# Performance work log

Measured on AMD Instinct MI355X. Metric: run time of the kernel, lower is better.

## Reference

```python
import jax, jax.numpy as jnp
import numpy as np

B, T, D, H = 2, 2048, 1024, 16
HD = D // H
DFF = 4 * D
EPS = 1e-5


def gelu_tanh(x):
    c = jnp.sqrt(2.0 / jnp.pi).astype(x.dtype)
    return 0.5 * x * (1.0 + jnp.tanh(c * (x + 0.044715 * x ** 3)))


def layernorm(x, scale, shift):
    mean = jnp.mean(x, axis=-1, keepdims=True)
    var = jnp.var(x, axis=-1, keepdims=True)  # unbiased=False
    return (x - mean) / jnp.sqrt(var + EPS) * scale + shift


def setup_inputs() -> dict:
    key = jax.random.key(0)
    ks = jax.random.split(key, 12)
    s = lambda fan_in: 1.0 / np.sqrt(fan_in)
    return {
        "x": jax.random.normal(ks[0], (B, T, D), jnp.float32),
        "wq": jax.random.normal(ks[1], (D, D), jnp.float32) * s(D),
        "wk": jax.random.normal(ks[2], (D, D), jnp.float32) * s(D),
        "wv": jax.random.normal(ks[3], (D, D), jnp.float32) * s(D),
        "wo": jax.random.normal(ks[4], (D, D), jnp.float32) * s(D),
        "bo": jnp.zeros((D,), jnp.float32),
        "ln1_scale": jnp.ones((D,), jnp.float32),
        "ln1_shift": jnp.zeros((D,), jnp.float32),
        "ln2_scale": jnp.ones((D,), jnp.float32),
        "ln2_shift": jnp.zeros((D,), jnp.float32),
        "w1": jax.random.normal(ks[5], (D, DFF), jnp.float32) * s(D),
        "b1": jnp.zeros((DFF,), jnp.float32),
        "w2": jax.random.normal(ks[6], (DFF, D), jnp.float32) * s(DFF),
        "b2": jnp.zeros((D,), jnp.float32),
    }


def reference(x, wq, wk, wv, wo, bo, ln1_scale, ln1_shift, ln2_scale, ln2_shift, w1, b1, w2, b2):
    # pre-LN attention
    h = layernorm(x, ln1_scale, ln1_shift)
    q = (h @ wq).reshape(B, T, H, HD).transpose(0, 2, 1, 3)  # [B,H,T,hd]
    k = (h @ wk).reshape(B, T, H, HD).transpose(0, 2, 1, 3)
    v = (h @ wv).reshape(B, T, H, HD).transpose(0, 2, 1, 3)
    scores = jnp.einsum('bhqd,bhkd->bhqk', q, k) / jnp.sqrt(jnp.float32(HD))
    causal = jnp.tril(jnp.ones((T, T), bool))
    scores = jnp.where(causal, scores, -jnp.inf)
    attn = jax.nn.softmax(scores, axis=-1)
    ctx = jnp.einsum('bhqk,bhkd->bhqd', attn, v)
    ctx = ctx.transpose(0, 2, 1, 3).reshape(B, T, D)
    attn_out = ctx @ wo + bo
    x = x + attn_out  # dropout p=0
    # pre-LN FFN
    h2 = layernorm(x, ln2_scale, ln2_shift)
    ff = gelu_tanh(h2 @ w1 + b1) @ w2 + b2
    return x + ff
```

## Files before the change

kernel.cpp:

```cpp
#include <hip/hip_runtime.h>
#include <hip/hip_bf16.h>
#include <stdint.h>

typedef unsigned short u16;
typedef __attribute__((ext_vector_type(8))) short s16x8;
typedef __attribute__((ext_vector_type(4))) float f32x4;

#define B_   2
#define T_   2048
#define D_   1024
#define H_   16
#define HD_  64
#define DFF_ 4096
#define M_   (B_*T_)

#define SC2F 0.18033688f

__device__ __forceinline__ u16 f2b(float f){
  uint32_t u = __float_as_uint(f);
  u += 0x7FFFu + ((u >> 16) & 1u);
  return (u16)(u >> 16);
}
__device__ __forceinline__ uint32_t pk2(float lo, float hi){
  uint32_t r;
  asm volatile("v_cvt_pk_bf16_f32 %0, %1, %2" : "=v"(r) : "v"(lo), "v"(hi));
  return r;
}

__device__ __forceinline__ void gl_lds16(const void* g, void* l){
  __builtin_amdgcn_global_load_lds((const __attribute__((address_space(1))) void*)g,
                                   (__attribute__((address_space(3))) void*)l, 16, 0, 0);
}

#define WAITV4 asm volatile("s_waitcnt vmcnt(4)" ::: "memory")
#define WAITV0 asm volatile("s_waitcnt vmcnt(0)" ::: "memory")
#define BARRIER do{ asm volatile("":::"memory"); __builtin_amdgcn_s_barrier(); \
                    asm volatile("":::"memory"); }while(0)

__global__ __launch_bounds__(256) void wconv_all(const float* __restrict__ wq,
                                                 const float* __restrict__ wk,
                                                 const float* __restrict__ wv,
                                                 const float* __restrict__ wo,
                                                 const float* __restrict__ w1,
                                                 const float* __restrict__ w2,
                                                 u16* __restrict__ wqkvT, u16* __restrict__ woT,
                                                 u16* __restrict__ w1T,   u16* __restrict__ w2T){
  const int bid = blockIdx.x;
  const float* W; u16* Wt; int K, N, tk, tn;
  if (bid < 1024){
    const int which = bid >> 8, t = bid & 255; tk = t >> 4; tn = t & 15; K = 1024; N = 1024;
    W  = (which == 0) ? wq : (which == 1) ? wk : (which == 2) ? wv : wo;
    Wt = (which == 3) ? woT : wqkvT + (size_t)which * D_ * D_;
  } else if (bid < 2048){
    const int t = bid - 1024; tk = t >> 6; tn = t & 63; K = 1024; N = 4096; W = w1; Wt = w1T;
  } else {
    const int t = bid - 2048; tk = t >> 4; tn = t & 15; K = 4096; N = 1024; W = w2; Wt = w2T;
  }
  const int k0 = tk << 6, n0 = tn << 6;
  __shared__ u16 tile[64][68];
  const int tid = threadIdx.x;
  const int rr = tid >> 4, c4 = (tid & 15) << 2;
  #pragma unroll
  for (int rep = 0; rep < 4; rep++){
    int r = rr + (rep << 4);
    float4 v = *reinterpret_cast<const float4*>(W + (size_t)(k0 + r)*N + n0 + c4);
    tile[r][c4+0] = f2b(v.x); tile[r][c4+1] = f2b(v.y);
    tile[r][c4+2] = f2b(v.z); tile[r][c4+3] = f2b(v.w);
  }
  __syncthreads();
  const int rn = tid >> 2, kb = (tid & 3) << 4;
  u16 tmp[16];
  #pragma unroll
  for (int j = 0; j < 16; j++) tmp[j] = tile[kb + j][rn];
  ushort4* dst = reinterpret_cast<ushort4*>(Wt + (size_t)(n0 + rn)*K + k0 + kb);
  dst[0] = make_ushort4(tmp[0], tmp[1], tmp[2], tmp[3]);
  dst[1] = make_ushort4(tmp[4], tmp[5], tmp[6], tmp[7]);
  dst[2] = make_ushort4(tmp[8], tmp[9], tmp[10], tmp[11]);
  dst[3] = make_ushort4(tmp[12], tmp[13], tmp[14], tmp[15]);
}

__global__ __launch_bounds__(256) void ln_kernel(const float* __restrict__ X,
                                                 const float* __restrict__ sc,
                                                 const float* __restrict__ sh,
                                                 u16* __restrict__ out){
  const int row = blockIdx.x;
  const int tid = threadIdx.x;
  float4 a = reinterpret_cast<const float4*>(X + ((size_t)row << 10))[tid];
  float s = a.x + a.y + a.z + a.w;
  float q = a.x*a.x + a.y*a.y + a.z*a.z + a.w*a.w;
  #pragma unroll
  for (int o = 32; o > 0; o >>= 1){ s += __shfl_xor(s, o); q += __shfl_xor(q, o); }
  __shared__ float red[8];
  const int w = tid >> 6;
  if ((tid & 63) == 0){ red[w] = s; red[4 + w] = q; }
  __syncthreads();
  float S = red[0] + red[1] + red[2] + red[3];
  float Q = red[4] + red[5] + red[6] + red[7];
  float mean = S * (1.0f/1024.0f);
  float var  = Q * (1.0f/1024.0f) - mean*mean;
  float inv = rsqrtf(var + 1e-5f);
  float4 gsc = reinterpret_cast<const float4*>(sc)[tid];
  float4 gsh = reinterpret_cast<const float4*>(sh)[tid];
  ushort4 o4;
  o4.x = f2b((a.x - mean)*inv*gsc.x + gsh.x);
  o4.y = f2b((a.y - mean)*inv*gsc.y + gsh.y);
  o4.z = f2b((a.z - mean)*inv*gsc.z + gsh.z);
  o4.w = f2b((a.w - mean)*inv*gsc.w + gsh.w);
  reinterpret_cast<ushort4*>(out + ((size_t)row << 10))[tid] = o4;
}

__global__ __launch_bounds__(256) void reduce2(const float* __restrict__ p,
                                               const float* __restrict__ bias,
                                               const float* __restrict__ resid,
                                               float* __restrict__ out){
  const size_t idx = ((size_t)blockIdx.x << 8) + threadIdx.x;
  float4 a = reinterpret_cast<const float4*>(p)[idx];
  float4 b = reinterpret_cast<const float4*>(p)[idx + (((size_t)M_*D_) >> 2)];
  float4 r = reinterpret_cast<const float4*>(resid)[idx];
  float4 bb = reinterpret_cast<const float4*>(bias)[threadIdx.x];
  float4 o;
  o.x = a.x + b.x + r.x + bb.x;
  o.y = a.y + b.y + r.y + bb.y;
  o.z = a.z + b.z + r.z + bb.z;
  o.w = a.w + b.w + r.w + bb.w;
  reinterpret_cast<float4*>(out)[idx] = o;
}

__global__ __launch_bounds__(256) void reduce_ln(const float* __restrict__ p,
                                                 const float* __restrict__ bias,
                                                 const float* __restrict__ resid,
                                                 const float* __restrict__ sc,
                                                 const float* __restrict__ sh,
                                                 float* __restrict__ x1,
                                                 u16* __restrict__ h2){
  const int row = blockIdx.x;
  const int tid = threadIdx.x;
  const size_t idx = ((size_t)row << 8) + tid;
  float4 a  = reinterpret_cast<const float4*>(p)[idx];
  float4 b  = reinterpret_cast<const float4*>(p)[idx + (((size_t)M_*D_) >> 2)];
  float4 r  = reinterpret_cast<const float4*>(resid)[idx];
  float4 bb = reinterpret_cast<const float4*>(bias)[tid];
  float4 v;
  v.x = a.x + b.x + r.x + bb.x;
  v.y = a.y + b.y + r.y + bb.y;
  v.z = a.z + b.z + r.z + bb.z;
  v.w = a.w + b.w + r.w + bb.w;
  reinterpret_cast<float4*>(x1)[idx] = v;
  float s = v.x + v.y + v.z + v.w;
  float q = v.x*v.x + v.y*v.y + v.z*v.z + v.w*v.w;
  #pragma unroll
  for (int o = 32; o > 0; o >>= 1){ s += __shfl_xor(s, o); q += __shfl_xor(q, o); }
  __shared__ float red[8];
  const int w = tid >> 6;
  if ((tid & 63) == 0){ red[w] = s; red[4 + w] = q; }
  __syncthreads();
  float S = red[0] + red[1] + red[2] + red[3];
  float Q = red[4] + red[5] + red[6] + red[7];
  float mean = S * (1.0f/1024.0f);
  float var  = Q * (1.0f/1024.0f) - mean*mean;
  float inv = rsqrtf(var + 1e-5f);
  float4 gsc = reinterpret_cast<const float4*>(sc)[tid];
  float4 gsh = reinterpret_cast<const float4*>(sh)[tid];
  ushort4 o4;
  o4.x = f2b((v.x - mean)*inv*gsc.x + gsh.x);
  o4.y = f2b((v.y - mean)*inv*gsc.y + gsh.y);
  o4.z = f2b((v.z - mean)*inv*gsc.z + gsh.z);
  o4.w = f2b((v.w - mean)*inv*gsc.w + gsh.w);
  reinterpret_cast<ushort4*>(h2 + ((size_t)row << 10))[tid] = o4;
}

template<int EPI>
__global__ __launch_bounds__(256) void gemm_k(const u16* __restrict__ A, const u16* __restrict__ Bt,
                                              const float* __restrict__ bias,
                                              void* __restrict__ Cv, int M, int N, int K, int lda){
  __shared__ __align__(16) u16 As[2][128*32];
  __shared__ __align__(16) u16 Bs[2][128*32];
  const int tid = threadIdx.x;
  const int lane = tid & 63;
  const int w = tid >> 6;
  const int wr = w >> 1, wc = w & 1;
  const int g = lane >> 4, l15 = lane & 15;

  const int nx = gridDim.x, ny = gridDim.y;
  const int nwg = nx * ny * gridDim.z;
  const int flat = blockIdx.x + nx * (blockIdx.y + ny * blockIdx.z);
  const int nf = (flat & 7) * (nwg >> 3) + (flat >> 3);
  const int tn = nf % nx;
  const int rest = nf / nx;
  const int tm = rest % ny;
  const int kz = rest / ny;
  const int tn0 = tn << 7;
  const int tm0 = tm << 7;
  const u16* Az = A  + (size_t)kz * K;
  const u16* Bz = Bt + (size_t)kz * K;

  f32x4 acc[4][4];
  #pragma unroll
  for (int i = 0; i < 4; i++)
    #pragma unroll
    for (int j = 0; j < 4; j++) acc[i][j] = (f32x4){0.f,0.f,0.f,0.f};

  const int ch0 = tid, ch1 = 256 + tid;
  const int r0 = ch0 >> 2, c0 = (((ch0 & 3) ^ ((r0 >> 1) & 3)) << 3);
  const int r1 = ch1 >> 2, c1 = (((ch1 & 3) ^ ((r1 >> 1) & 3)) << 3);
  const u16* A0 = Az + (size_t)(tm0 + r0)*lda + c0;
  const u16* A1 = Az + (size_t)(tm0 + r1)*lda + c1;
  const u16* B0 = Bz + (size_t)(tn0 + r0)*lda + c0;
  const u16* B1 = Bz + (size_t)(tn0 + r1)*lda + c1;

#define GSTAGE(BUF, TI) do {                         \
    const int off_ = (TI) << 5;                      \
    gl_lds16(A0 + off_, As[BUF] + ch0*8);            \
    gl_lds16(A1 + off_, As[BUF] + ch1*8);            \
    gl_lds16(B0 + off_, Bs[BUF] + ch0*8);            \
    gl_lds16(B1 + off_, Bs[BUF] + ch1*8);            \
  } while(0)

#define GCOMP(BUF) do {                                                                   \
    s16x8 af[4], bf[4];                                                                   \
    _Pragma("unroll")                                                                     \
    for (int i = 0; i < 4; i++){                                                          \
      int ra = (wr << 6) + (i << 4) + l15;                                                \
      af[i] = *reinterpret_cast<const s16x8*>(As[BUF] + ra*32 + ((g ^ ((ra >> 1) & 3)) << 3)); \
    }                                                                                     \
    _Pragma("unroll")                                                                     \
    for (int j = 0; j < 4; j++){                                                          \
      int rb = (wc << 6) + (j << 4) + l15;                                                \
      bf[j] = *reinterpret_cast<const s16x8*>(Bs[BUF] + rb*32 + ((g ^ ((rb >> 1) & 3)) << 3)); \
    }                                                                                     \
    _Pragma("unroll")                                                                     \
    for (int i = 0; i < 4; i++)                                                           \
      _Pragma("unroll")                                                                   \
      for (int j = 0; j < 4; j++)                                                         \
        acc[i][j] = __builtin_amdgcn_mfma_f32_16x16x32_bf16(af[i], bf[j], acc[i][j], 0, 0, 0); \
  } while(0)

  const int NT = K >> 5;
  GSTAGE(0, 0);
  for (int t = 0; t < NT; t += 2){
    if (t + 1 < NT) { GSTAGE(1, t + 1); WAITV4; } else { WAITV0; }
    BARRIER;
    GCOMP(0);
    BARRIER;
    if (t + 2 < NT) { GSTAGE(0, t + 2); WAITV4; } else { WAITV0; }
    BARRIER;
    GCOMP(1);
    BARRIER;
  }
#undef GSTAGE
#undef GCOMP

  #pragma unroll
  for (int i = 0; i < 4; i++){
    const int mb = tm0 + (wr << 6) + (i << 4) + (g << 2);
    #pragma unroll
    for (int j = 0; j < 4; j++){
      const int n = tn0 + (wc << 6) + (j << 4) + l15;
      #pragma unroll
      for (int rr = 0; rr < 4; rr++){
        const int m = mb + rr;
        float v = acc[i][j][rr];
        if constexpr (EPI == 0){
          ((float*)Cv)[(size_t)kz*((size_t)M*N) + (size_t)m*N + n] = v;
        } else if constexpr (EPI == 1){
          const int sel = n >> 10, nn = n & 1023;
          const int hh = nn >> 6, d = nn & 63;
          if (sel == 0) v *= SC2F;
          ((u16*)Cv)[(size_t)sel*((size_t)M_*D_) +
                     ((((size_t)(m >> 11)*H_ + hh)*T_ + (m & 2047)) << 6) + d] = f2b(v);
        } else {
          float u = v + bias[n];
          float t2 = 0.7978845608f*(u + 0.044715f*u*u*u);
          float e = __expf(2.0f*t2);
          float th = 1.0f - 2.0f/(e + 1.0f);
          ((u16*)Cv)[(size_t)m*N + n] = f2b(0.5f*u*(1.0f + th));
        }
      }
    }
  }
}

__global__ __launch_bounds__(256) void attn_k(const u16* __restrict__ Qg, const u16* __restrict__ Kg,
                                              const u16* __restrict__ Vg, u16* __restrict__ ctx){
  const int flat = blockIdx.x + (blockIdx.y << 4);
  const int xcd = flat & 7, j_ = flat >> 3;
  const int bh  = ((j_ & 3) << 3) + xcd;
  const int pr_ = j_ >> 2;
  const int tid = threadIdx.x;
  const int lane = tid & 63;
  const int w = tid >> 6;
  const int g = lane >> 4, l15 = lane & 15;

  __shared__ __align__(16) u16 Qs[64*64];
  __shared__ __align__(16) u16 Ks[2][64*64];
  __shared__ __align__(16) u16 Vt[2][64*64];
  __shared__ __align__(16) u16 Pl[4][16*64];

  const size_t hb = (size_t)bh * ((size_t)T_*HD_);
  const u16* Qh = Qg + hb;
  const u16* Kh = Kg + hb;
  const u16* Vh = Vg + hb;
  const int b = bh >> 4, hh = bh & 15;

  const int s_r0 = tid >> 3,        s_c0 = (((tid & 7) ^ (s_r0 & 7)) << 3);
  const int s_r1 = (256+tid) >> 3,  s_c1 = ((((256+tid) & 7) ^ (s_r1 & 7)) << 3);
  const int v_kr = tid >> 2, v_d0 = (tid & 3) << 4;

#define SINK_V(buf, q0, q1, q2, q3) do {                                          \
    u16 vv[16] = {q0.x,q0.y,q0.z,q0.w, q1.x,q1.y,q1.z,q1.w,                       \
                  q2.x,q2.y,q2.z,q2.w, q3.x,q3.y,q3.z,q3.w};                      \
    _Pragma("unroll")                                                             \
    for (int j = 0; j < 16; j++){                                                 \
      int d = v_d0 + j;                                                           \
      Vt[buf][d*64 + ((((v_kr >> 3) ^ (d & 7) ^ ((d >> 4) << 1)) & 7) << 3)       \
              + (v_kr & 7)] = vv[j];                                              \
    }                                                                             \
  } while (0)

  for (int ph = 0; ph < 2; ++ph){
    const int qt = ph ? (31 - pr_) : pr_;

    gl_lds16(Qh + (size_t)(qt*64 + s_r0)*HD_ + s_c0, Qs + tid*8);
    gl_lds16(Qh + (size_t)(qt*64 + s_r1)*HD_ + s_c1, Qs + (256+tid)*8);
    gl_lds16(Kh + (size_t)(s_r0)*HD_ + s_c0, Ks[0] + tid*8);
    gl_lds16(Kh + (size_t)(s_r1)*HD_ + s_c1, Ks[0] + (256+tid)*8);
    {
      const u16* vs = Vh + (size_t)v_kr*HD_ + v_d0;
      ushort4 a0 = *(const ushort4*)(vs + 0);
      ushort4 a1 = *(const ushort4*)(vs + 4);
      ushort4 a2 = *(const ushort4*)(vs + 8);
      ushort4 a3 = *(const ushort4*)(vs + 12);
      SINK_V(0, a0, a1, a2, a3);
    }
    __syncthreads();

    s16x8 qa[2];
    #pragma unroll
    for (int kk = 0; kk < 2; kk++){
      int ra = (w << 4) + l15;
      int slot = (kk << 2) + g;
      qa[kk] = *reinterpret_cast<const s16x8*>(Qs + ra*64 + ((slot ^ (ra & 7)) << 3));
    }

    f32x4 accO[4];
    #pragma unroll
    for (int j = 0; j < 4; j++) accO[j] = (f32x4){0.f,0.f,0.f,0.f};
    float mrow = -1e30f, lrow = 0.f;
    const int qlt = (w << 4) + l15;

    for (int kt = 0; kt <= qt; ++kt){
      const int cur = kt & 1, nxt = cur ^ 1;
      const bool pf = (kt < qt);

      ushort4 p0, p1, p2, p3;
      if (pf){
        gl_lds16(Kh + (size_t)((kt+1)*64 + s_r0)*HD_ + s_c0, Ks[nxt] + tid*8);
        gl_lds16(Kh + (size_t)((kt+1)*64 + s_r1)*HD_ + s_c1, Ks[nxt] + (256+tid)*8);
        const u16* vs = Vh + (size_t)((kt+1)*64 + v_kr)*HD_ + v_d0;
        p0 = *(const ushort4*)(vs + 0);
        p1 = *(const ushort4*)(vs + 4);
        p2 = *(const ushort4*)(vs + 8);
        p3 = *(const ushort4*)(vs + 12);
      }

      f32x4 accS[4];
      #pragma unroll
      for (int j = 0; j < 4; j++) accS[j] = (f32x4){0.f,0.f,0.f,0.f};
      __builtin_amdgcn_s_setprio(1);
      #pragma unroll
      for (int jn = 0; jn < 4; jn++){
        #pragma unroll
        for (int kk = 0; kk < 2; kk++){
          int rb = (jn << 4) + l15;
          int slot = (kk << 2) + g;
          s16x8 kf = *reinterpret_cast<const s16x8*>(Ks[cur] + rb*64 + ((slot ^ (rb & 7)) << 3));
          accS[jn] = __builtin_amdgcn_mfma_f32_16x16x32_bf16(kf, qa[kk], accS[jn], 0, 0, 0);
        }
      }
      __builtin_amdgcn_s_setprio(0);

      float sv[4][4];
      #pragma unroll
      for (int jn = 0; jn < 4; jn++)
        #pragma unroll
        for (int rr = 0; rr < 4; rr++){
          float xv = accS[jn][rr];
          if (kt == qt){
            int kl = (jn << 4) + (g << 2) + rr;
            if (kl > qlt) xv = -1e30f;
          }
          sv[jn][rr] = xv;
        }

      float rmax = sv[0][0];
      #pragma unroll
      for (int jn = 0; jn < 4; jn++)
        #pragma unroll
        for (int rr = 0; rr < 4; rr++) rmax = fmaxf(rmax, sv[jn][rr]);
      rmax = fmaxf(rmax, __shfl_xor(rmax, 16));
      rmax = fmaxf(rmax, __shfl_xor(rmax, 32));

      if (__any(rmax > mrow + 8.0f)){
        float mn = fmaxf(mrow, rmax);
        float sf = exp2f(mrow - mn);
        mrow = mn;
        lrow *= sf;
        #pragma unroll
        for (int rr = 0; rr < 4; rr++){
          float sfr = __shfl(sf, ((lane >> 4) << 2) + rr);
          #pragma unroll
          for (int jn = 0; jn < 4; jn++) accO[jn][rr] *= sfr;
        }
      }

      float tsum = 0.f;
      #pragma unroll
      for (int jn = 0; jn < 4; jn++){
        float pv0 = exp2f(sv[jn][0] - mrow);
        float pv1 = exp2f(sv[jn][1] - mrow);
        float pv2 = exp2f(sv[jn][2] - mrow);
        float pv3 = exp2f(sv[jn][3] - mrow);
        tsum += (pv0 + pv1) + (pv2 + pv3);
        int slot = (jn << 1) | (g >> 1);
        int base = l15*64 + (((slot ^ (l15 & 7)) & 7) << 3) + ((g & 1) << 2);
        uint2 pkd = make_uint2(pk2(pv0, pv1), pk2(pv2, pv3));
        *reinterpret_cast<uint2*>(&Pl[w][base]) = pkd;
      }
      tsum += __shfl_xor(tsum, 16);
      tsum += __shfl_xor(tsum, 32);
      lrow += tsum;

      __builtin_amdgcn_s_setprio(1);
      #pragma unroll
      for (int kk = 0; kk < 2; kk++){
        int slot = (kk << 2) + g;
        s16x8 pa = *reinterpret_cast<const s16x8*>(
            &Pl[w][l15*64 + (((slot ^ (l15 & 7)) & 7) << 3)]);
        #pragma unroll
        for (int jn = 0; jn < 4; jn++){
          int vd = (jn << 4) + l15;
          s16x8 vbf = *reinterpret_cast<const s16x8*>(
              Vt[cur] + vd*64 + (((slot ^ (vd & 7) ^ ((vd >> 4) << 1)) & 7) << 3));
          accO[jn] = __builtin_amdgcn_mfma_f32_16x16x32_bf16(pa, vbf, accO[jn], 0, 0, 0);
        }
      }
      __builtin_amdgcn_s_setprio(0);

      if (pf) SINK_V(nxt, p0, p1, p2, p3);
      __syncthreads();
    }

    #pragma unroll
    for (int rr = 0; rr < 4; rr++){
      float lr = __shfl(lrow, ((lane >> 4) << 2) + rr);
      float inv = 1.0f / lr;
      int qrow = qt*64 + (w << 4) + (g << 2) + rr;
      size_t rowbase = ((size_t)(b*T_ + qrow) << 10) + ((size_t)hh << 6);
      #pragma unroll
      for (int jn = 0; jn < 4; jn++){
        int d = (jn << 4) + l15;
        ctx[rowbase + d] = f2b(accO[jn][rr] * inv);
      }
    }
  }
#undef SINK_V
}

extern "C" void kernel_launch(void* const* d_in, const int* in_sizes, int n_in,
                              void* d_out, int out_size, void* d_ws, size_t ws_size,
                              hipStream_t stream){
  (void)in_sizes; (void)n_in; (void)out_size; (void)ws_size;
  const float* x    = (const float*)d_in[0];
  const float* wq   = (const float*)d_in[1];
  const float* wk   = (const float*)d_in[2];
  const float* wv   = (const float*)d_in[3];
  const float* wo   = (const float*)d_in[4];
  const float* bo   = (const float*)d_in[5];
  const float* ln1s = (const float*)d_in[6];
  const float* ln1b = (const float*)d_in[7];
  const float* ln2s = (const float*)d_in[8];
  const float* ln2b = (const float*)d_in[9];
  const float* w1   = (const float*)d_in[10];
  const float* b1   = (const float*)d_in[11];
  const float* w2   = (const float*)d_in[12];
  const float* b2   = (const float*)d_in[13];
  float* out = (float*)d_out;

  char* p = (char*)d_ws;
  u16*  wqkvT = (u16*)p;  p += (size_t)3*D_*D_*2;
  u16*  woT   = (u16*)p;  p += (size_t)D_*D_*2;
  u16*  w1T   = (u16*)p;  p += (size_t)D_*DFF_*2;
  u16*  w2T   = (u16*)p;  p += (size_t)DFF_*D_*2;
  u16*  h     = (u16*)p;  p += (size_t)M_*D_*2;
  u16*  qb    = (u16*)p;  p += (size_t)M_*D_*2;
  u16*  kb    = (u16*)p;  p += (size_t)M_*D_*2;
  u16*  vb    = (u16*)p;  p += (size_t)M_*D_*2;
  u16*  ctx   = (u16*)p;  p += (size_t)M_*D_*2;
  float* x1   = (float*)p; p += (size_t)M_*D_*4;
  u16*  h2    = (u16*)p;  p += (size_t)M_*D_*2;
  u16*  ff1   = (u16*)p;  p += (size_t)M_*DFF_*2;
  (void)kb; (void)vb;
  float* part = (float*)h;

  dim3 blk(256);
  wconv_all<<<3072, blk, 0, stream>>>(wq, wk, wv, wo, w1, w2, wqkvT, woT, w1T, w2T);
  ln_kernel<<<M_, blk, 0, stream>>>(x, ln1s, ln1b, h);
  gemm_k<1><<<dim3(24,32,1), blk, 0, stream>>>(h, wqkvT, nullptr, qb, M_, 3*D_, D_, D_);
  attn_k<<<dim3(16,32), blk, 0, stream>>>(qb, qb + (size_t)M_*D_, qb + 2*(size_t)M_*D_, ctx);
  gemm_k<0><<<dim3(8,32,2), blk, 0, stream>>>(ctx, woT, nullptr, part, M_, D_, D_/2, D_);
  reduce_ln<<<M_, blk, 0, stream>>>(part, bo, x, ln2s, ln2b, x1, h2);
  gemm_k<3><<<dim3(32,32,1), blk, 0, stream>>>(h2, w1T, b1, ff1, M_, DFF_, D_, D_);
  gemm_k<0><<<dim3(8,32,2), blk, 0, stream>>>(ff1, w2T, nullptr, part, M_, D_, DFF_/2, DFF_);
  reduce2<<<M_, blk, 0, stream>>>(part, b2, x1, out);
}
```

Measured before the change: 252.8 us.

## Replace GEMM with 8-wave 256-row tile kernel using phased LDS pipelining

Replaces the 256-thread 128x128 GEMM with a 512-thread kernel that computes 256xN tiles (N=256 or 128, depending on the template). It uses a 64-wide K step with double-buffered LDS and an XOR swizzle, and splits each K step into phases. Each phase loads A fragments, issues the next global→LDS stage, synchronises, then runs MFMAs at raised priority. The goal is more data reuse per tile, fewer barriers per unit of MFMA work, and load latency hidden behind compute. The cost is higher register and LDS pressure and fewer workgroups per launch, which may leave CUs idle on the smaller GEMMs.

After: 239.5 us. 1.06x faster.

```diff
diff --git a/kernel.cpp b/kernel.cpp
--- a/kernel.cpp
+++ b/kernel.cpp
@@ -32,10 +32,11 @@
                                    (__attribute__((address_space(3))) void*)l, 16, 0, 0);
 }
 
-#define WAITV4 asm volatile("s_waitcnt vmcnt(4)" ::: "memory")
-#define WAITV0 asm volatile("s_waitcnt vmcnt(0)" ::: "memory")
-#define BARRIER do{ asm volatile("":::"memory"); __builtin_amdgcn_s_barrier(); \
-                    asm volatile("":::"memory"); }while(0)
+template<int N> __device__ __forceinline__ void waitvm(){
+  if constexpr (N == 0)      asm volatile("s_waitcnt vmcnt(0)" ::: "memory");
+  else if constexpr (N == 2) asm volatile("s_waitcnt vmcnt(2)" ::: "memory");
+  else                       asm volatile("s_waitcnt vmcnt(4)" ::: "memory");
+}
 
 __global__ __launch_bounds__(256) void wconv_all(const float* __restrict__ wq,
                                                  const float* __restrict__ wk,
@@ -169,97 +170,120 @@
   reinterpret_cast<ushort4*>(h2 + ((size_t)row << 10))[tid] = o4;
 }
 
-template<int EPI>
-__global__ __launch_bounds__(256) void gemm_k(const u16* __restrict__ A, const u16* __restrict__ Bt,
-                                              const float* __restrict__ bias,
-                                              void* __restrict__ Cv, int M, int N, int K, int lda){
-  __shared__ __align__(16) u16 As[2][128*32];
-  __shared__ __align__(16) u16 Bs[2][128*32];
+template<int EPI, int NF>
+__global__ __launch_bounds__(512, 2) void gemm8(const u16* __restrict__ A, const u16* __restrict__ Bt,
+                                                const float* __restrict__ bias,
+                                                void* __restrict__ Cv, int M, int N, int K, int lda){
+  constexpr int BROWS = NF * 32;
+  __shared__ __align__(16) u16 LA[2][2][128*64];
+  __shared__ __align__(16) u16 LB[2][2][BROWS*64];
   const int tid = threadIdx.x;
   const int lane = tid & 63;
   const int w = tid >> 6;
-  const int wr = w >> 1, wc = w & 1;
+  const int wm = w >> 2, wn = w & 3;
   const int g = lane >> 4, l15 = lane & 15;
+  const int bnb = (wn & 1) * (NF * 16);
 
   const int nx = gridDim.x, ny = gridDim.y;
   const int nwg = nx * ny * gridDim.z;
   const int flat = blockIdx.x + nx * (blockIdx.y + ny * blockIdx.z);
-  const int nf = (flat & 7) * (nwg >> 3) + (flat >> 3);
-  const int tn = nf % nx;
-  const int rest = nf / nx;
+  const int nfid = (flat & 7) * (nwg >> 3) + (flat >> 3);
+  const int tn = nfid % nx;
+  const int rest = nfid / nx;
   const int tm = rest % ny;
   const int kz = rest / ny;
-  const int tn0 = tn << 7;
-  const int tm0 = tm << 7;
+  const int tn0 = tn * (NF * 64);
+  const int tm0 = tm << 8;
   const u16* Az = A  + (size_t)kz * K;
   const u16* Bz = Bt + (size_t)kz * K;
 
-  f32x4 acc[4][4];
+  const int arow0 = tid >> 3,         asl0 = (((tid) & 7) ^ (arow0 & 7)) << 3;
+  const int arow1 = (tid + 512) >> 3, asl1 = (((tid + 512) & 7) ^ (arow1 & 7)) << 3;
+
+  f32x4 acc[8][NF];
   #pragma unroll
-  for (int i = 0; i < 4; i++)
+  for (int i = 0; i < 8; i++)
     #pragma unroll
-    for (int j = 0; j < 4; j++) acc[i][j] = (f32x4){0.f,0.f,0.f,0.f};
-
-  const int ch0 = tid, ch1 = 256 + tid;
-  const int r0 = ch0 >> 2, c0 = (((ch0 & 3) ^ ((r0 >> 1) & 3)) << 3);
-  const int r1 = ch1 >> 2, c1 = (((ch1 & 3) ^ ((r1 >> 1) & 3)) << 3);
-  const u16* A0 = Az + (size_t)(tm0 + r0)*lda + c0;
-  const u16* A1 = Az + (size_t)(tm0 + r1)*lda + c1;
-  const u16* B0 = Bz + (size_t)(tn0 + r0)*lda + c0;
-  const u16* B1 = Bz + (size_t)(tn0 + r1)*lda + c1;
-
-#define GSTAGE(BUF, TI) do {                         \
-    const int off_ = (TI) << 5;                      \
-    gl_lds16(A0 + off_, As[BUF] + ch0*8);            \
-    gl_lds16(A1 + off_, As[BUF] + ch1*8);            \
-    gl_lds16(B0 + off_, Bs[BUF] + ch0*8);            \
-    gl_lds16(B1 + off_, Bs[BUF] + ch1*8);            \
-  } while(0)
-
-#define GCOMP(BUF) do {                                                                   \
-    s16x8 af[4], bf[4];                                                                   \
-    _Pragma("unroll")                                                                     \
-    for (int i = 0; i < 4; i++){                                                          \
-      int ra = (wr << 6) + (i << 4) + l15;                                                \
-      af[i] = *reinterpret_cast<const s16x8*>(As[BUF] + ra*32 + ((g ^ ((ra >> 1) & 3)) << 3)); \
-    }                                                                                     \
-    _Pragma("unroll")                                                                     \
-    for (int j = 0; j < 4; j++){                                                          \
-      int rb = (wc << 6) + (j << 4) + l15;                                                \
-      bf[j] = *reinterpret_cast<const s16x8*>(Bs[BUF] + rb*32 + ((g ^ ((rb >> 1) & 3)) << 3)); \
-    }                                                                                     \
-    _Pragma("unroll")                                                                     \
-    for (int i = 0; i < 4; i++)                                                           \
-      _Pragma("unroll")                                                                   \
-      for (int j = 0; j < 4; j++)                                                         \
-        acc[i][j] = __builtin_amdgcn_mfma_f32_16x16x32_bf16(af[i], bf[j], acc[i][j], 0, 0, 0); \
-  } while(0)
-
-  const int NT = K >> 5;
-  GSTAGE(0, 0);
+    for (int j = 0; j < NF; j++) acc[i][j] = (f32x4){0.f,0.f,0.f,0.f};
+  s16x8 bf[NF][2];
+
+#define STG_A(db, h, tt) do{                                                        \
+    gl_lds16(Az + (size_t)(tm0 + (h)*128 + arow0)*lda + ((tt) << 6) + asl0,         \
+             &LA[db][h][tid*8]);                                                    \
+    gl_lds16(Az + (size_t)(tm0 + (h)*128 + arow1)*lda + ((tt) << 6) + asl1,         \
+             &LA[db][h][(tid + 512)*8]);                                            \
+  }while(0)
+#define STG_B(db, h, tt) do{                                                        \
+    gl_lds16(Bz + (size_t)(tn0 + (h)*BROWS + arow0)*lda + ((tt) << 6) + asl0,       \
+             &LB[db][h][tid*8]);                                                    \
+    if constexpr (NF == 4){                                                         \
+      gl_lds16(Bz + (size_t)(tn0 + (h)*BROWS + arow1)*lda + ((tt) << 6) + asl1,     \
+               &LB[db][h][(tid + 512)*8]);                                          \
+    }                                                                               \
+  }while(0)
+#define LDAF(db, mf, kk) (*reinterpret_cast<const s16x8*>(                          \
+    &LA[db][wm][((mf)*16 + l15)*64 + ((((kk)*4 + g) ^ (l15 & 7)) << 3)]))
+#define LDBF(db, nf, kk) (*reinterpret_cast<const s16x8*>(                          \
+    &LB[db][wn >> 1][(bnb + (nf)*16 + l15)*64 + ((((kk)*4 + g) ^ (l15 & 7)) << 3)]))
+#define BLOAD(db) do{ _Pragma("unroll")                                             \
+    for (int nf = 0; nf < NF; nf++){ bf[nf][0] = LDBF(db, nf, 0);                   \
+                                     bf[nf][1] = LDBF(db, nf, 1); } }while(0)
+#define PH(db, MFA, MFB, STG, WV) do{                                               \
+    s16x8 a00 = LDAF(db, MFA, 0), a01 = LDAF(db, MFA, 1);                           \
+    s16x8 a10 = LDAF(db, MFB, 0), a11 = LDAF(db, MFB, 1);                           \
+    STG;                                                                            \
+    WV;                                                                             \
+    __builtin_amdgcn_s_barrier();                                                   \
+    __builtin_amdgcn_s_setprio(1);                                                  \
+    _Pragma("unroll")                                                               \
+    for (int nf = 0; nf < NF; nf++){                                                \
+      acc[MFA][nf] = __builtin_amdgcn_mfma_f32_16x16x32_bf16(a00, bf[nf][0], acc[MFA][nf], 0,0,0); \
+      acc[MFA][nf] = __builtin_amdgcn_mfma_f32_16x16x32_bf16(a01, bf[nf][1], acc[MFA][nf], 0,0,0); \
+      acc[MFB][nf] = __builtin_amdgcn_mfma_f32_16x16x32_bf16(a10, bf[nf][0], acc[MFB][nf], 0,0,0); \
+      acc[MFB][nf] = __builtin_amdgcn_mfma_f32_16x16x32_bf16(a11, bf[nf][1], acc[MFB][nf], 0,0,0); \
+    }                                                                               \
+    __builtin_amdgcn_s_setprio(0);                                                  \
+    __builtin_amdgcn_s_barrier();                                                   \
+  }while(0)
+
+  const int NT = K >> 6;
+  STG_B(0, 0, 0); STG_B(0, 1, 0); STG_A(0, 0, 0); STG_A(0, 1, 0);
+  STG_B(1, 0, 1); STG_B(1, 1, 1);
+  waitvm<NF>();
+  __builtin_amdgcn_s_barrier();
+
   for (int t = 0; t < NT; t += 2){
-    if (t + 1 < NT) { GSTAGE(1, t + 1); WAITV4; } else { WAITV0; }
-    BARRIER;
-    GCOMP(0);
-    BARRIER;
-    if (t + 2 < NT) { GSTAGE(0, t + 2); WAITV4; } else { WAITV0; }
-    BARRIER;
-    GCOMP(1);
-    BARRIER;
+    const bool last = (t + 2 >= NT);
+    BLOAD(0);
+    PH(0, 0, 1, STG_A(1, 0, t + 1), );
+    PH(0, 2, 3, STG_A(1, 1, t + 1), );
+    PH(0, 4, 5, if (!last) STG_B(0, 0, t + 2), );
+    PH(0, 6, 7, if (!last) STG_B(0, 1, t + 2),
+                if (last) waitvm<0>(); else waitvm<NF>(););
+    BLOAD(1);
+    PH(1, 0, 1, if (!last) STG_A(0, 0, t + 2), );
+    PH(1, 2, 3, if (!last) STG_A(0, 1, t + 2), );
+    PH(1, 4, 5, if (!last) STG_B(1, 0, t + 3), );
+    PH(1, 6, 7, if (!last) STG_B(1, 1, t + 3),
+                if (last) waitvm<0>(); else waitvm<NF>(););
   }
-#undef GSTAGE
-#undef GCOMP
+#undef STG_A
+#undef STG_B
+#undef LDAF
+#undef LDBF
+#undef BLOAD
+#undef PH
 
   #pragma unroll
-  for (int i = 0; i < 4; i++){
-    const int mb = tm0 + (wr << 6) + (i << 4) + (g << 2);
+  for (int mf = 0; mf < 8; mf++){
+    const int mb = tm0 + wm*128 + mf*16 + (g << 2);
     #pragma unroll
-    for (int j = 0; j < 4; j++){
-      const int n = tn0 + (wc << 6) + (j << 4) + l15;
+    for (int nf = 0; nf < NF; nf++){
+      const int n = tn0 + wn*(NF*16) + nf*16 + l15;
       #pragma unroll
       for (int rr = 0; rr < 4; rr++){
         const int m = mb + rr;
-        float v = acc[i][j][rr];
+        float v = acc[mf][nf][rr];
         if constexpr (EPI == 0){
           ((float*)Cv)[(size_t)kz*((size_t)M*N) + (size_t)m*N + n] = v;
         } else if constexpr (EPI == 1){
@@ -502,14 +526,14 @@
   (void)kb; (void)vb;
   float* part = (float*)h;
 
-  dim3 blk(256);
+  dim3 blk(256), blk8(512);
   wconv_all<<<3072, blk, 0, stream>>>(wq, wk, wv, wo, w1, w2, wqkvT, woT, w1T, w2T);
   ln_kernel<<<M_, blk, 0, stream>>>(x, ln1s, ln1b, h);
-  gemm_k<1><<<dim3(24,32,1), blk, 0, stream>>>(h, wqkvT, nullptr, qb, M_, 3*D_, D_, D_);
+  gemm8<1,4><<<dim3(12,16,1), blk8, 0, stream>>>(h, wqkvT, nullptr, qb, M_, 3*D_, D_, D_);
   attn_k<<<dim3(16,32), blk, 0, stream>>>(qb, qb + (size_t)M_*D_, qb + 2*(size_t)M_*D_, ctx);
-  gemm_k<0><<<dim3(8,32,2), blk, 0, stream>>>(ctx, woT, nullptr, part, M_, D_, D_/2, D_);
+  gemm8<0,2><<<dim3(8,16,2), blk8, 0, stream>>>(ctx, woT, nullptr, part, M_, D_, D_/2, D_);
   reduce_ln<<<M_, blk, 0, stream>>>(part, bo, x, ln2s, ln2b, x1, h2);
-  gemm_k<3><<<dim3(32,32,1), blk, 0, stream>>>(h2, w1T, b1, ff1, M_, DFF_, D_, D_);
-  gemm_k<0><<<dim3(8,32,2), blk, 0, stream>>>(ff1, w2T, nullptr, part, M_, D_, DFF_/2, DFF_);
+  gemm8<3,4><<<dim3(16,16,1), blk8, 0, stream>>>(h2, w1T, b1, ff1, M_, DFF_, D_, D_);
+  gemm8<0,2><<<dim3(8,16,2), blk8, 0, stream>>>(ff1, w2T, nullptr, part, M_, D_, DFF_/2, DFF_);
   reduce2<<<M_, blk, 0, stream>>>(part, b2, x1, out);
 }
```
